# Performance work log

Hardware: AMD Instinct MI355X
Metric: run time of the kernel (lower is better)

Reference implementation:

```python
import jax, jax.numpy as jnp
import numpy as np

H = 128   # hidden_dim
E = 768   # embedding_dim
L = 20    # num_layers
B = 64    # batch
T = 512   # seq_len


def setup_inputs() -> dict:
    key = jax.random.key(0)
    ks = jax.random.split(key, 9)
    k = 1.0 / np.sqrt(H)  # PyTorch LSTM default init scale
    u = lambda kk, shape: jax.random.uniform(kk, shape, jnp.float32, -k, k)
    return {
        "x": jax.random.normal(ks[0], (B, T, E), jnp.float32),
        "Wih0": u(ks[1], (4 * H, E)),        # layer 0 input weights
        "Whh0": u(ks[2], (4 * H, H)),
        "bih0": u(ks[3], (4 * H,)),
        "bhh0": u(ks[4], (4 * H,)),
        "Wih": u(ks[5], (L - 1, 4 * H, H)),  # layers 1..19
        "Whh": u(ks[6], (L - 1, 4 * H, H)),
        "bih": u(ks[7], (L - 1, 4 * H)),
        "bhh": u(ks[8], (L - 1, 4 * H)),
    }


def _lstm_layer(xs, Wih, Whh, b):
    # xs: [T, B, Din] -> ys: [T, B, H], h_final: [B, H]
    bsz = xs.shape[1]
    pre = jnp.einsum('tbd,gd->tbg', xs, Wih) + b  # precompute input projections

    def step(carry, pt):
        h, c = carry
        g = pt + h @ Whh.T  # [B, 4H]
        i, f, gg, o = jnp.split(g, 4, axis=-1)  # PyTorch gate order i,f,g,o
        i = jax.nn.sigmoid(i)
        f = jax.nn.sigmoid(f)
        gg = jnp.tanh(gg)
        o = jax.nn.sigmoid(o)
        c = f * c + i * gg
        h = o * jnp.tanh(c)
        return (h, c), h

    init = (jnp.zeros((bsz, H), xs.dtype), jnp.zeros((bsz, H), xs.dtype))
    (_, _), ys = jax.lax.scan(step, init, pre)
    return ys, ys[-1]


def reference(x, Wih0, Whh0, bih0, bhh0, Wih, Whh, bih, bhh):
    xs = jnp.swapaxes(x, 0, 1)  # [T, B, E]
    ys, _ = _lstm_layer(xs, Wih0, Whh0, bih0 + bhh0)

    def layer_fn(ys, params):
        Wl, Wh, bi, bh = params
        ys2, h = _lstm_layer(ys, Wl, Wh, bi + bh)
        return ys2, h

    ys, hs = jax.lax.scan(layer_fn, ys, (Wih, Whh, bih, bhh))
    return hs[-1]  # hidden state of last (20th) layer at final timestep: [B, H]
```

## Files before the change

kernel.cpp:

```cpp
#include <hip/hip_runtime.h>

#define H4 128
#define EE 768
#define NL 20
#define BB 64
#define TT 512
#define G4 512
#define NBG 8
#define CK 16
#define NCH (TT/CK)
#define RC 2

typedef _Float16 v8h __attribute__((ext_vector_type(8)));
typedef _Float16 v4h __attribute__((ext_vector_type(4)));
typedef float v4f __attribute__((ext_vector_type(4)));
typedef unsigned int v4u __attribute__((ext_vector_type(4)));
typedef unsigned int v2u __attribute__((ext_vector_type(2)));

#if defined(__has_builtin)
#if __has_builtin(__builtin_amdgcn_exp2f) && __has_builtin(__builtin_amdgcn_rcpf)
#define EXP2F __builtin_amdgcn_exp2f
#define RCPF  __builtin_amdgcn_rcpf
#endif
#endif
#ifndef EXP2F
#define EXP2F exp2f
#define RCPF(x) (1.0f/(x))
#endif

__device__ __forceinline__ float fast_sig(float x) {
  float e = EXP2F(-1.44269504f * x);
  return RCPF(1.0f + e);
}
__device__ __forceinline__ float fast_tanh(float x) {
  float e = EXP2F(2.88539008f * x);
  return 1.0f - 2.0f * RCPF(1.0f + e);
}

__device__ __forceinline__ int swz(int row, int byteInRow) {
  return (row * 256 + byteInRow) ^ ((row & 7) << 4);
}

__global__ __launch_bounds__(256) void prep_kernel(
    const float* __restrict__ Wih0, const float* __restrict__ Whh0,
    const float* __restrict__ bih,  const float* __restrict__ bhh,
    const float* __restrict__ Wih,  const float* __restrict__ Whh,
    _Float16* __restrict__ W0h, _Float16* __restrict__ Wc,
    float* __restrict__ biasc, unsigned* __restrict__ flags)
{
  long idx = (long)blockIdx.x * 256 + threadIdx.x;
  const long NWC = (long)NL * G4 * 256;
  const long NW0 = (long)G4 * EE;
  const long NBI = (long)NL * G4;
  if (idx < NWC) {
    int l = (int)(idx >> 17);
    int rem = (int)(idx & 131071);
    int n = rem >> 8, kk = rem & 255;
    float v;
    if (l == 0) v = (kk < 128) ? 0.0f : Whh0[n * H4 + kk - 128];
    else v = (kk < 128) ? Wih[((long)(l-1) * G4 + n) * H4 + kk]
                        : Whh[((long)(l-1) * G4 + n) * H4 + kk - 128];
    Wc[idx] = (_Float16)v;
  } else if ((idx -= NWC) < NW0) {
    W0h[idx] = (_Float16)Wih0[idx];
  } else if ((idx -= NW0) < NBI) {
    int l = (int)(idx >> 9), n = (int)(idx & 511);
    biasc[idx] = (l == 0) ? 0.0f : (bih[(l-1) * G4 + n] + bhh[(l-1) * G4 + n]);
  } else if ((idx -= NBI) < 256) {
    flags[idx] = 0u;
  }
}

__global__ __launch_bounds__(512) void pre0_gemm(
    const float* __restrict__ x, const _Float16* __restrict__ W0h,
    const float* __restrict__ bih0, const float* __restrict__ bhh0,
    _Float16* __restrict__ pre0)
{
  __shared__ __align__(16) unsigned char smem[46080];
  _Float16* sA = (_Float16*)smem;
  _Float16* sB = (_Float16*)(smem + 5120);
  _Float16* sC = (_Float16*)smem;
  int t = blockIdx.x;
  int tid = threadIdx.x;
  int w = tid >> 6, lane = tid & 63;
  int l15 = lane & 15, kb = lane >> 4;

  v4f acc[4][4];
#pragma unroll
  for (int mi = 0; mi < 4; ++mi)
#pragma unroll
    for (int ni = 0; ni < 4; ++ni) acc[mi][ni] = (v4f){0.f, 0.f, 0.f, 0.f};

  int bA = tid >> 3, kqA = tid & 7;
  const float* xp = x + ((long)bA * TT + t) * EE + kqA * 4;
  const _Float16* wp = W0h + (long)tid * EE;

  for (int k0 = 0; k0 < EE; k0 += 32) {
    float4 xv = *(const float4*)(xp + k0);
    v4h xh = { (_Float16)xv.x, (_Float16)xv.y, (_Float16)xv.z, (_Float16)xv.w };
    *(v4h*)&sA[bA * 40 + kqA * 4] = xh;
#pragma unroll
    for (int c = 0; c < 4; ++c)
      *(v8h*)&sB[tid * 40 + c * 8] = *(const v8h*)(wp + k0 + c * 8);
    __syncthreads();
#pragma unroll
    for (int mi = 0; mi < 4; ++mi) {
      v8h a = *(const v8h*)&sA[(16 * mi + l15) * 40 + kb * 8];
#pragma unroll
      for (int ni = 0; ni < 4; ++ni) {
        v8h b = *(const v8h*)&sB[(64 * w + 16 * ni + l15) * 40 + kb * 8];
        acc[mi][ni] = __builtin_amdgcn_mfma_f32_16x16x32_f16(a, b, acc[mi][ni], 0, 0, 0);
      }
    }
    __syncthreads();
  }

#pragma unroll
  for (int hh2 = 0; hh2 < 2; ++hh2) {
    __syncthreads();
    if ((w >> 2) == hh2) {
      int wl = w & 3;
#pragma unroll
      for (int ni = 0; ni < 4; ++ni) {
        int nloc = 64 * wl + 16 * ni + l15;
        int n = 256 * hh2 + nloc;
        float bia = bih0[n] + bhh0[n];
#pragma unroll
        for (int mi = 0; mi < 4; ++mi)
#pragma unroll
          for (int r = 0; r < 4; ++r)
            sC[nloc * 72 + 16 * mi + 4 * kb + r] = (_Float16)(acc[mi][ni][r] + bia);
      }
    }
    __syncthreads();
    int row = tid >> 1, part = tid & 1;
    _Float16* po = pre0 + ((long)t * G4 + 256 * hh2 + row) * 64 + part * 32;
#pragma unroll
    for (int c = 0; c < 4; ++c)
      *(v8h*)(po + c * 8) = *(const v8h*)&sC[row * 72 + part * 32 + c * 8];
  }
}

__global__ __launch_bounds__(512, 2) void lstm_pipe(
    const _Float16* __restrict__ pre0, const _Float16* __restrict__ Wc,
    const float* __restrict__ biasc, _Float16* __restrict__ yring,
    unsigned* __restrict__ flags, float* __restrict__ out)
{
  __shared__ __align__(16) unsigned char lds[40960];
  const int l = blockIdx.x >> 3, bg = blockIdx.x & 7;
  const int tid = threadIdx.x, w = tid >> 6, lane = tid & 63;
  const int l15 = lane & 15, kb = lane >> 4;
  const int jloc = 16 * w + l15;
  const bool valid = (kb < 2);
  const int b0 = 4 * (kb & 1);

  v8h bw[4][8];
  const _Float16* wbase = Wc + (long)l * G4 * 256;
#pragma unroll
  for (int q = 0; q < 4; ++q)
#pragma unroll
    for (int ks = 0; ks < 8; ++ks)
      bw[q][ks] = *(const v8h*)(wbase + (long)(128 * q + jloc) * 256 + ks * 32 + kb * 8);

  float bias_q[4];
#pragma unroll
  for (int q = 0; q < 4; ++q)
    bias_q[q] = (l == 0) ? 0.0f : biasc[l * G4 + 128 * q + jloc];

  *(v4u*)(lds + 32768 + tid * 16) = (v4u){0u, 0u, 0u, 0u};

  const int myf = l * 8 + bg;
  const unsigned* fin  = flags + ((l > 0) ? (myf - 8) : myf);
  const unsigned* fout = flags + ((l < NL - 1) ? (myf + 8) : myf);
  unsigned* fme = flags + myf;
  _Float16* ywr = yring + (long)myf * (RC * CK * 1024);
  const _Float16* yrd = yring + (long)(myf - 8) * (RC * CK * 1024);

  v4f cst = (v4f){0.f, 0.f, 0.f, 0.f};
  v4h pc[4];
  if (l == 0) {
    const _Float16* pb = pre0 + bg * 8 + b0;
#pragma unroll
    for (int q = 0; q < 4; ++q)
      pc[q] = *(const v4h*)(pb + (long)(128 * q + jloc) * 64);
  }

  __syncthreads();

  for (int c = 0; c < NCH; ++c) {
    if (l > 0) {
      unsigned f;
      for (;;) {
        asm volatile("global_load_dword %0, %1, off sc0 sc1\n\ts_waitcnt vmcnt(0)"
                     : "=v"(f) : "v"(fin));
        if (f > (unsigned)c) break;
        __builtin_amdgcn_s_sleep(2);
      }
      const _Float16* src = yrd + ((long)(c & (RC - 1)) * CK + (tid >> 5)) * 1024 + (tid & 31) * 32;
      v4u d0, d1, d2, d3;
      asm volatile("global_load_dwordx4 %0, %4, off sc0 sc1\n\t"
                   "global_load_dwordx4 %1, %4, off offset:16 sc0 sc1\n\t"
                   "global_load_dwordx4 %2, %4, off offset:32 sc0 sc1\n\t"
                   "global_load_dwordx4 %3, %4, off offset:48 sc0 sc1\n\t"
                   "s_waitcnt vmcnt(0)"
                   : "=v"(d0), "=v"(d1), "=v"(d2), "=v"(d3) : "v"(src));
      unsigned char* tb = lds + (tid >> 5) * 2048;
      const int j0 = (tid & 31) * 4;
      union { v4u u; _Float16 h[8]; } qq;
#pragma unroll
      for (int jj = 0; jj < 4; ++jj) {
        qq.u = (jj == 0) ? d0 : (jj == 1) ? d1 : (jj == 2) ? d2 : d3;
#pragma unroll
        for (int b = 0; b < 8; ++b)
          *(_Float16*)(tb + swz(b, (j0 + jj) * 2)) = qq.h[b];
      }
    }
    if (l < NL - 1 && c >= RC) {
      unsigned f;
      for (;;) {
        asm volatile("global_load_dword %0, %1, off sc0 sc1\n\ts_waitcnt vmcnt(0)"
                     : "=v"(f) : "v"(fout));
        if (f >= (unsigned)(c - 1)) break;
        __builtin_amdgcn_s_sleep(2);
      }
    }
    __syncthreads();

    for (int ts = 0; ts < CK; ++ts) {
      const int t = c * CK + ts;
      const int p = t & 1;
      v4f acc[4];
#pragma unroll
      for (int q = 0; q < 4; ++q)
        acc[q] = (v4f){bias_q[q], bias_q[q], bias_q[q], bias_q[q]};

      v4h pn[4];
      if (l == 0) {
#pragma unroll
        for (int q = 0; q < 4; ++q)
#pragma unroll
          for (int r = 0; r < 4; ++r) acc[q][r] += (float)pc[q][r];
        const int tn = (t + 1) & (TT - 1);
        const _Float16* pb = pre0 + (long)tn * G4 * 64 + bg * 8 + b0;
#pragma unroll
        for (int q = 0; q < 4; ++q)
          pn[q] = *(const v4h*)(pb + (long)(128 * q + jloc) * 64);
      }

      const unsigned char* hb = lds + 32768 + p * 4096;
      if (l > 0) {
        const unsigned char* yb = lds + ts * 2048;
#pragma unroll
        for (int ks = 0; ks < 4; ++ks) {
          v8h a = *(const v8h*)(yb + swz(l15, ks * 64 + kb * 16));
#pragma unroll
          for (int q = 0; q < 4; ++q)
            acc[q] = __builtin_amdgcn_mfma_f32_16x16x32_f16(a, bw[q][ks], acc[q], 0, 0, 0);
        }
      }
#pragma unroll
      for (int ks = 4; ks < 8; ++ks) {
        v8h a = *(const v8h*)(hb + swz(l15, (ks - 4) * 64 + kb * 16));
#pragma unroll
        for (int q = 0; q < 4; ++q)
          acc[q] = __builtin_amdgcn_mfma_f32_16x16x32_f16(a, bw[q][ks], acc[q], 0, 0, 0);
      }

      _Float16 hh[4]; float hf[4];
#pragma unroll
      for (int r = 0; r < 4; ++r) {
        float i_ = fast_sig(acc[0][r]);
        float f_ = fast_sig(acc[1][r]);
        float g_ = fast_tanh(acc[2][r]);
        float o_ = fast_sig(acc[3][r]);
        float cn = f_ * cst[r] + i_ * g_;
        cst[r] = cn;
        float h_ = o_ * fast_tanh(cn);
        hf[r] = h_; hh[r] = (_Float16)h_;
      }

      if (valid) {
        unsigned char* hn = lds + 32768 + (p ^ 1) * 4096;
#pragma unroll
        for (int r = 0; r < 4; ++r)
          *(_Float16*)(hn + swz(b0 + r, jloc * 2)) = hh[r];
        if (l < NL - 1) {
          union { v2u u; _Float16 h[4]; } pk;
#pragma unroll
          for (int r = 0; r < 4; ++r) pk.h[r] = hh[r];
          _Float16* dst = ywr + ((long)(c & (RC - 1)) * CK + ts) * 1024 + jloc * 8 + b0;
          asm volatile("global_store_dwordx2 %0, %1, off sc0 sc1" :: "v"(dst), "v"(pk.u));
        } else if (t == TT - 1) {
#pragma unroll
          for (int r = 0; r < 4; ++r)
            out[(bg * 8 + b0 + r) * H4 + jloc] = hf[r];
        }
      }
      if (l == 0) {
#pragma unroll
        for (int q = 0; q < 4; ++q) pc[q] = pn[q];
      }
      __syncthreads();
    }

    asm volatile("s_waitcnt vmcnt(0)" ::: "memory");
    __syncthreads();
    if (tid == 0) {
      unsigned v = (unsigned)(c + 1);
      asm volatile("global_store_dword %0, %1, off sc0 sc1" :: "v"(fme), "v"(v) : "memory");
    }
  }
}

extern "C" void kernel_launch(void* const* d_in, const int* in_sizes, int n_in,
                              void* d_out, int out_size, void* d_ws, size_t ws_size,
                              hipStream_t stream)
{
  const float* x    = (const float*)d_in[0];
  const float* Wih0 = (const float*)d_in[1];
  const float* Whh0 = (const float*)d_in[2];
  const float* bih0 = (const float*)d_in[3];
  const float* bhh0 = (const float*)d_in[4];
  const float* Wih  = (const float*)d_in[5];
  const float* Whh  = (const float*)d_in[6];
  const float* bih  = (const float*)d_in[7];
  const float* bhh  = (const float*)d_in[8];
  float* out = (float*)d_out;
  char* ws = (char*)d_ws;

  _Float16* pre0  = (_Float16*)(ws);
  _Float16* W0h   = (_Float16*)(ws + 33554432);
  _Float16* Wc    = (_Float16*)(ws + 34340864);
  float*    bc    = (float*)   (ws + 39583744);
  _Float16* yring = (_Float16*)(ws + 39624704);
  unsigned* flags = (unsigned*)(ws + 50110464);

  prep_kernel<<<11817, 256, 0, stream>>>(Wih0, Whh0, bih, bhh, Wih, Whh, W0h, Wc, bc, flags);
  pre0_gemm<<<TT, 512, 0, stream>>>(x, W0h, bih0, bhh0, pre0);
  lstm_pipe<<<NL * NBG, 512, 0, stream>>>(pre0, Wc, bc, yring, flags, out);
}
```

Before: 1.150 ms.

## Store inter-layer ring in swizzled LDS layout for direct vector copy

The producer now writes each hidden value into the global ring buffer using the consumer's swizzled LDS layout, with 2-byte stores. The consumer can then copy a chunk with four 16-byte loads and four 16-byte LDS stores, replacing the per-halfword scatter. Launch bounds drop to one block per SM, and an empty asm pins the weight registers so they stay resident. The trade-off is four narrow global stores per step instead of one 8-byte store, which puts more store traffic on the recurrent critical path.

```diff
diff --git a/kernel.cpp b/kernel.cpp
--- a/kernel.cpp
+++ b/kernel.cpp
@@ -15,7 +15,6 @@
 typedef _Float16 v4h __attribute__((ext_vector_type(4)));
 typedef float v4f __attribute__((ext_vector_type(4)));
 typedef unsigned int v4u __attribute__((ext_vector_type(4)));
-typedef unsigned int v2u __attribute__((ext_vector_type(2)));
 
 #if defined(__has_builtin)
 #if __has_builtin(__builtin_amdgcn_exp2f) && __has_builtin(__builtin_amdgcn_rcpf)
@@ -141,7 +140,7 @@
   }
 }
 
-__global__ __launch_bounds__(512, 2) void lstm_pipe(
+__global__ __launch_bounds__(512, 1) void lstm_pipe(
     const _Float16* __restrict__ pre0, const _Float16* __restrict__ Wc,
     const float* __restrict__ biasc, _Float16* __restrict__ yring,
     unsigned* __restrict__ flags, float* __restrict__ out)
@@ -161,6 +160,11 @@
 #pragma unroll
     for (int ks = 0; ks < 8; ++ks)
       bw[q][ks] = *(const v8h*)(wbase + (long)(128 * q + jloc) * 256 + ks * 32 + kb * 8);
+#pragma unroll
+  for (int q = 0; q < 4; ++q)
+#pragma unroll
+    for (int ks = 0; ks < 8; ++ks)
+      asm volatile("" : "+v"(bw[q][ks]));
 
   float bias_q[4];
 #pragma unroll
@@ -173,8 +177,8 @@
   const unsigned* fin  = flags + ((l > 0) ? (myf - 8) : myf);
   const unsigned* fout = flags + ((l < NL - 1) ? (myf + 8) : myf);
   unsigned* fme = flags + myf;
-  _Float16* ywr = yring + (long)myf * (RC * CK * 1024);
-  const _Float16* yrd = yring + (long)(myf - 8) * (RC * CK * 1024);
+  char* ywr = (char*)(yring + (long)myf * (RC * CK * 1024));
+  const char* yrd = (const char*)(yring + (long)(myf - 8) * (RC * CK * 1024));
 
   v4f cst = (v4f){0.f, 0.f, 0.f, 0.f};
   v4h pc[4];
@@ -196,24 +200,19 @@
         if (f > (unsigned)c) break;
         __builtin_amdgcn_s_sleep(2);
       }
-      const _Float16* src = yrd + ((long)(c & (RC - 1)) * CK + (tid >> 5)) * 1024 + (tid & 31) * 32;
+      const char* src = yrd + (long)(c & (RC - 1)) * 32768 + tid * 16;
       v4u d0, d1, d2, d3;
-      asm volatile("global_load_dwordx4 %0, %4, off sc0 sc1\n\t"
-                   "global_load_dwordx4 %1, %4, off offset:16 sc0 sc1\n\t"
-                   "global_load_dwordx4 %2, %4, off offset:32 sc0 sc1\n\t"
-                   "global_load_dwordx4 %3, %4, off offset:48 sc0 sc1\n\t"
-                   "s_waitcnt vmcnt(0)"
-                   : "=v"(d0), "=v"(d1), "=v"(d2), "=v"(d3) : "v"(src));
-      unsigned char* tb = lds + (tid >> 5) * 2048;
-      const int j0 = (tid & 31) * 4;
-      union { v4u u; _Float16 h[8]; } qq;
-#pragma unroll
-      for (int jj = 0; jj < 4; ++jj) {
-        qq.u = (jj == 0) ? d0 : (jj == 1) ? d1 : (jj == 2) ? d2 : d3;
-#pragma unroll
-        for (int b = 0; b < 8; ++b)
-          *(_Float16*)(tb + swz(b, (j0 + jj) * 2)) = qq.h[b];
-      }
+      asm volatile("global_load_dwordx4 %0, %1, off sc0 sc1" : "=v"(d0) : "v"(src));
+      asm volatile("global_load_dwordx4 %0, %1, off sc0 sc1" : "=v"(d1) : "v"(src + 8192));
+      asm volatile("global_load_dwordx4 %0, %1, off sc0 sc1" : "=v"(d2) : "v"(src + 16384));
+      asm volatile("global_load_dwordx4 %0, %1, off sc0 sc1" : "=v"(d3) : "v"(src + 24576));
+      asm volatile("s_waitcnt vmcnt(0)" ::: "memory");
+      __builtin_amdgcn_sched_barrier(0);
+      unsigned char* dst = lds + tid * 16;
+      *(v4u*)(dst)         = d0;
+      *(v4u*)(dst +  8192) = d1;
+      *(v4u*)(dst + 16384) = d2;
+      *(v4u*)(dst + 24576) = d3;
     }
     if (l < NL - 1 && c >= RC) {
       unsigned f;
@@ -285,11 +284,15 @@
         for (int r = 0; r < 4; ++r)
           *(_Float16*)(hn + swz(b0 + r, jloc * 2)) = hh[r];
         if (l < NL - 1) {
-          union { v2u u; _Float16 h[4]; } pk;
-#pragma unroll
-          for (int r = 0; r < 4; ++r) pk.h[r] = hh[r];
-          _Float16* dst = ywr + ((long)(c & (RC - 1)) * CK + ts) * 1024 + jloc * 8 + b0;
-          asm volatile("global_store_dwordx2 %0, %1, off sc0 sc1" :: "v"(dst), "v"(pk.u));
+          char* dstb = ywr + (long)(c & (RC - 1)) * 32768 + ts * 2048;
+#pragma unroll
+          for (int r = 0; r < 4; ++r) {
+            union { _Float16 h; unsigned short u; } cv; cv.h = hh[r];
+            unsigned val = cv.u;
+            char* dst = dstb + swz(b0 + r, jloc * 2);
+            asm volatile("global_store_short %0, %1, off sc0 sc1"
+                         :: "v"(dst), "v"(val) : "memory");
+          }
         } else if (t == TT - 1) {
 #pragma unroll
           for (int r = 0; r < 4; ++r)
```

Measured after the change: 1.181 ms. 2.7% more time.
